# Kernel tuning notes

Hardware: AMD Instinct MI355X
Metric: run time of the kernel (lower is better)

The kernel has to match this reference:

```python
import jax, jax.numpy as jnp
import numpy as np

B, S, L = 32, 50, 16            # batch, seq_len, lectures per step
C, D = 50, 64                   # num_concepts, hidden_dim (key=value=summary dim)
NQ, NL, NU = 10000, 2000, 5000  # num_items, num_nonassessed_items, num_users
QV = NQ + NL + 1                # q_embed vocab (questions + lectures + pad)
QAV = 2 * NQ + 1                # qa_embed vocab
H4 = 4 * D                      # linear_dim = 4 * value_dim
EPS = 1e-5                      # torch LayerNorm default eps


def setup_inputs() -> dict:
    ks = jax.random.split(jax.random.key(0), 16)
    rn = lambda k, sh, sc: jax.random.normal(k, sh, jnp.float32) * sc
    return dict(
        q_data=jax.random.randint(ks[0], (B, S), 0, QV),
        qa_data=jax.random.randint(ks[1], (B, S), 0, QAV),
        l_data=jax.random.randint(ks[2], (B, S, L), 0, QV),
        users=jax.random.randint(ks[3], (B,), 0, NU + 1),
        key_matrix=rn(ks[4], (C, D), (2.0 / D) ** 0.5),   # key_matrix_embed rows 1..C (kaiming)
        q_embed=rn(ks[5], (QV, D), 0.02),
        qa_embed=rn(ks[6], (QAV, D), 0.02),
        u_embed=rn(ks[7], (NU + 1, D), 0.02),             # looked up but unused by write()
        M0=rn(ks[8], (C, D), (2.0 / D) ** 0.5),           # kaiming-init value matrix
        W_e=rn(ks[9], (D, D), D ** -0.5), b_e=jnp.zeros((D,), jnp.float32),
        W_a=rn(ks[10], (D, D), D ** -0.5), b_a=jnp.zeros((D,), jnp.float32),
        ln_gamma=jnp.ones((H4,), jnp.float32), ln_beta=jnp.zeros((H4,), jnp.float32),
        W0=rn(ks[11], (H4, H4), H4 ** -0.5), b0=jnp.zeros((H4,), jnp.float32),
        W1=rn(ks[12], (H4, H4), H4 ** -0.5), b1=jnp.zeros((H4,), jnp.float32),
        W_out=rn(ks[13], (H4, 1), H4 ** -0.5), b_out=jnp.zeros((1,), jnp.float32),
    )


def _forward(q_data, qa_data, l_data, key_matrix, q_embed, qa_embed, M0,
             W_e, b_e, W_a, b_a, ln_gamma, ln_beta, W0, b0, W1, b1, W_out, b_out):
    Bv = q_data.shape[0]
    q_e = q_embed[q_data]        # (B,S,D)
    qa_e = qa_embed[qa_data]     # (B,S,D)
    l_e = q_embed[l_data]        # (B,S,L,D) lectures share the q embedding table

    corr = lambda x: jax.nn.softmax(x @ key_matrix.T, axis=-1)  # softmax addressing
    q_cw = corr(q_e)             # (B,S,C)
    l_cw = corr(l_e)             # (B,S,L,C)
    # erase / add gates are memory-independent -> precompute (batched GEMMs)
    l_er = jax.nn.sigmoid(l_e @ W_e + b_e); l_ad = jnp.tanh(l_e @ W_a + b_a)
    q_er = jax.nn.sigmoid(qa_e @ W_e + b_e); q_ad = jnp.tanh(qa_e @ W_a + b_a)

    tm2 = lambda x: jnp.swapaxes(x, 0, 1)           # (B,S,..) -> (S,B,..)
    tm3 = lambda x: jnp.transpose(x, (1, 2, 0, 3))  # (B,S,L,..) -> (S,L,B,..)
    xs = (tm2(q_cw), tm2(q_e), tm2(q_er), tm2(q_ad),
          tm3(l_cw), tm3(l_e), tm3(l_er), tm3(l_ad))

    def write(M, w, e, a):  # erase-add gated write
        w = w[:, :, None]   # (B,C,1)
        return M * (1.0 - w * e[:, None, :]) + w * a[:, None, :]

    def layer_norm(x):
        mu = jnp.mean(x, -1, keepdims=True)
        v = jnp.var(x, -1, keepdims=True)
        return (x - mu) * jax.lax.rsqrt(v + EPS) * ln_gamma + ln_beta

    def outer(M, step):
        qcw, q, qer, qad, lcw, le, ler, lad = step
        q_read = jnp.einsum('bc,bcd->bd', qcw, M)  # read BEFORE lecture writes

        def inner(carry, lx):
            Mc, acc = carry
            w, e, a = lx
            acc = acc + jnp.einsum('bc,bcd->bd', w, Mc)  # read then write
            return (write(Mc, w, e, a), acc), None

        (M, l_read), _ = jax.lax.scan(inner, (M, jnp.zeros_like(q)), (lcw, ler, lad))
        # `l` after the loop is the LAST lecture embedding of this step
        mastery = layer_norm(jnp.concatenate([q_read, q, l_read, le[-1]], axis=-1))
        h = jax.nn.relu(mastery @ W0 + b0) @ W1 + b1   # dropout = identity (eval)
        pred = jax.nn.sigmoid(h @ W_out + b_out)[:, 0]
        M = write(M, qcw, qer, qad)                    # commit the q/a interaction
        return M, pred

    M_init = jnp.broadcast_to(M0, (Bv,) + M0.shape)
    _, preds = jax.lax.scan(outer, M_init, xs)
    return jnp.swapaxes(preds, 0, 1)                   # (B,S)


def reference(q_data, qa_data, l_data, users, key_matrix, q_embed, qa_embed,
              u_embed, M0, W_e, b_e, W_a, b_a, ln_gamma, ln_beta,
              W0, b0, W1, b1, W_out, b_out):
    # users/u_embed are looked up by the torch module but unused by write()'s math
    return _forward(q_data, qa_data, l_data, key_matrix, q_embed, qa_embed, M0,
                    W_e, b_e, W_a, b_a, ln_gamma, ln_beta, W0, b0, W1, b1, W_out, b_out)
```

## Files before the change

kernel.cpp:

```cpp
#include <hip/hip_runtime.h>
#include <math.h>

#define BB 32
#define SS 50
#define LL 16
#define CC 50
#define DD 64
#define NCH 13
#define H4 256
#define NROWS_Q (BB*SS)
#define NROWS_L (BB*SS*LL)

#define EA_ST 2176
#define W_ST  68

#define RB 64
#define NBLK_L (NROWS_L/RB)
#define NBLK_Q (NROWS_Q/RB)
#define NGB (NBLK_L + 2*NBLK_Q)

#define KBAT 16
#define NBAT (H4/KBAT)

static_assert(EA_ST == 17*128, "ea record: 17 slots x 64 lanes x float2");
static_assert(W_ST == 17*4, "w record: 17 slots x 4 chunk-cols");
static_assert(SS % 2 == 0, "phaseA double-step pipeline needs even SS");
static_assert(NROWS_L % RB == 0 && NROWS_Q % RB == 0, "GEMM row blocking");
static_assert(NBAT*KBAT == H4 && NBAT % 2 == 0,
              "phaseB k-loop must cover ALL of H4 in pairs of batches");
static_assert(SS*DD % 4 == 0, "phaseA partial copy uses float4");

#define OFF_EA     ((size_t)0)
#define OFF_W      (OFF_EA + (size_t)NROWS_Q*EA_ST)
#define OFF_PQP    (OFF_W  + (size_t)BB*NCH*SS*W_ST)
#define OFF_PLP    (OFF_PQP + (size_t)NCH*BB*SS*DD)
#define OFF_QE     (OFF_PLP + (size_t)NCH*BB*SS*DD)
#define OFF_LELAST (OFF_QE + (size_t)NROWS_Q*DD)

__global__ __launch_bounds__(256, 4) void k0_kernel(
    const int* __restrict__ qd, const int* __restrict__ qadx,
    const int* __restrict__ ld,
    const float* __restrict__ Kmat, const float* __restrict__ qemb,
    const float* __restrict__ qaemb,
    const float* __restrict__ We, const float* __restrict__ Wa,
    const float* __restrict__ be, const float* __restrict__ ba,
    float* __restrict__ eaW, float* __restrict__ wrecW,
    float* __restrict__ q_e_o, float* __restrict__ le_last)
{
    __shared__ float sX[RB*DD];
    __shared__ float sW[32*192];

    int tid = threadIdx.x;
    int bid = blockIdx.x;

    int bt, base;
    if (bid < NBLK_L)              { bt = 0; base = bid*RB; }
    else if (bid < NBLK_L+NBLK_Q)  { bt = 1; base = (bid-NBLK_L)*RB; }
    else                           { bt = 2; base = (bid-NBLK_L-NBLK_Q)*RB; }

    {
        const int*   idsrc = (bt==0) ? ld : (bt==1) ? qd : qadx;
        const float* tab   = (bt==2) ? qaemb : qemb;
        for (int idx = tid; idx < RB*16; idx += 256) {
            int r = idx >> 4, q = idx & 15;
            int id = idsrc[base + r];
            *(float4*)(sX + r*64 + q*4) =
                *(const float4*)(tab + (size_t)id*DD + q*4);
        }
    }

    auto stageW = [&](int kb) {
        #pragma unroll
        for (int n = 0; n < 4; ++n) {
            int f  = n*256 + tid;
            int kl = f >> 5, cf = f & 31;
            int k  = kb + kl;
            const float* src = (cf < 16) ? (We + k*64 + cf*4)
                                         : (Wa + k*64 + (cf-16)*4);
            *(float4*)(sW + kl*192 + cf*4) = *(const float4*)src;
        }
        #pragma unroll
        for (int n = 0; n < 8; ++n) {
            int f  = n*256 + tid;
            int kl = f >> 6, cr = f & 63;
            int k  = kb + kl;
            sW[kl*192 + 128 + cr] = (cr < CC) ? Kmat[cr*64 + k] : 0.f;
        }
    };

    int lane = tid & 63, wvi = tid >> 6;
    int r0 = wvi * 16;

    float accE[16], accA[16], accS[16];
    #pragma unroll
    for (int r = 0; r < 16; ++r) { accE[r] = 0.f; accA[r] = 0.f; accS[r] = 0.f; }

    stageW(0);
    __syncthreads();

    #pragma unroll 2
    for (int k4 = 0; k4 < 8; ++k4) {
        float wE[4], wA4[4], wS[4];
        #pragma unroll
        for (int kk = 0; kk < 4; ++kk) {
            int krow = (k4*4 + kk)*192;
            wE[kk]  = sW[krow + lane];
            wA4[kk] = sW[krow + 64 + lane];
            wS[kk]  = sW[krow + 128 + lane];
        }
        #pragma unroll
        for (int r = 0; r < 16; ++r) {
            float4 xv = *(const float4*)(sX + (r0+r)*64 + k4*4);
            accE[r] = fmaf(xv.x, wE[0], accE[r]);
            accE[r] = fmaf(xv.y, wE[1], accE[r]);
            accE[r] = fmaf(xv.z, wE[2], accE[r]);
            accE[r] = fmaf(xv.w, wE[3], accE[r]);
            accA[r] = fmaf(xv.x, wA4[0], accA[r]);
            accA[r] = fmaf(xv.y, wA4[1], accA[r]);
            accA[r] = fmaf(xv.z, wA4[2], accA[r]);
            accA[r] = fmaf(xv.w, wA4[3], accA[r]);
            accS[r] = fmaf(xv.x, wS[0], accS[r]);
            accS[r] = fmaf(xv.y, wS[1], accS[r]);
            accS[r] = fmaf(xv.z, wS[2], accS[r]);
            accS[r] = fmaf(xv.w, wS[3], accS[r]);
        }
    }
    __syncthreads();

    stageW(32);
    __syncthreads();

    #pragma unroll 2
    for (int k4 = 0; k4 < 8; ++k4) {
        float wE[4], wA4[4], wS[4];
        #pragma unroll
        for (int kk = 0; kk < 4; ++kk) {
            int krow = (k4*4 + kk)*192;
            wE[kk]  = sW[krow + lane];
            wA4[kk] = sW[krow + 64 + lane];
            wS[kk]  = sW[krow + 128 + lane];
        }
        #pragma unroll
        for (int r = 0; r < 16; ++r) {
            float4 xv = *(const float4*)(sX + (r0+r)*64 + 32 + k4*4);
            accE[r] = fmaf(xv.x, wE[0], accE[r]);
            accE[r] = fmaf(xv.y, wE[1], accE[r]);
            accE[r] = fmaf(xv.z, wE[2], accE[r]);
            accE[r] = fmaf(xv.w, wE[3], accE[r]);
            accA[r] = fmaf(xv.x, wA4[0], accA[r]);
            accA[r] = fmaf(xv.y, wA4[1], accA[r]);
            accA[r] = fmaf(xv.z, wA4[2], accA[r]);
            accA[r] = fmaf(xv.w, wA4[3], accA[r]);
            accS[r] = fmaf(xv.x, wS[0], accS[r]);
            accS[r] = fmaf(xv.y, wS[1], accS[r]);
            accS[r] = fmaf(xv.z, wS[2], accS[r]);
            accS[r] = fmaf(xv.w, wS[3], accS[r]);
        }
    }

    float bev = be[lane], bav = ba[lane];

    #pragma unroll
    for (int r = 0; r < 16; ++r) {
        int rr = r0 + r;
        int grow = base + rr;

        float s = (lane < CC) ? accS[r] : -1e30f;
        float mx = s;
        #pragma unroll
        for (int o = 32; o >= 1; o >>= 1) mx = fmaxf(mx, __shfl_xor(mx, o));
        float p = (lane < CC) ? expf(s - mx) : 0.f;
        float sum = p;
        #pragma unroll
        for (int o = 32; o >= 1; o >>= 1) sum += __shfl_xor(sum, o);
        float wsm = p / sum;

        if (bt == 0) {
            float erv = 1.f / (1.f + expf(-(accE[r] + bev)));
            float adv = tanhf(accA[r] + bav);
            int bs = grow >> 4, il = grow & 15;
            *(float2*)(eaW + (size_t)bs*EA_ST + il*128 + lane*2) =
                make_float2(erv, adv);
            int b = bs / SS, s2 = bs - b*SS;
            if (lane < 52) {
                int omx = lane >> 2, j = lane & 3;
                wrecW[(((size_t)(b*NCH + omx)*SS + s2)*17 + il)*4 + j] =
                    (lane < CC) ? wsm : 0.f;
            }
            if (il == LL-1) le_last[(size_t)bs*DD + lane] = sX[rr*64 + lane];
        } else if (bt == 1) {
            int qrow = grow;
            int b = qrow / SS, s2 = qrow - b*SS;
            if (lane < 52) {
                int omx = lane >> 2, j = lane & 3;
                wrecW[(((size_t)(b*NCH + omx)*SS + s2)*17 + 16)*4 + j] =
                    (lane < CC) ? wsm : 0.f;
            }
            q_e_o[(size_t)qrow*DD + lane] = sX[rr*64 + lane];
        } else {
            float erv = 1.f / (1.f + expf(-(accE[r] + bev)));
            float adv = tanhf(accA[r] + bav);
            int qrow = grow;
            *(float2*)(eaW + (size_t)qrow*EA_ST + 2048 + lane*2) =
                make_float2(erv, adv);
        }
    }
}

__global__ __launch_bounds__(64) void phaseA_kernel(
    const float* __restrict__ M0,
    const float* __restrict__ ea, const float* __restrict__ wrec,
    float* __restrict__ PqP, float* __restrict__ PlP)
{
    int om   = blockIdx.x >> 5;
    int b    = blockIdx.x & 31;
    int lane = threadIdx.x;
    int c0   = om * 4;

    __shared__ __align__(16) float wbuf[2][W_ST];
    __shared__ __align__(16) float sPq[SS*DD];
    __shared__ __align__(16) float sPl[SS*DD];

    float M[4];
    #pragma unroll
    for (int i = 0; i < 4; ++i) {
        int c = c0 + i;
        M[i] = (c < CC) ? M0[c*DD + lane] : 0.f;
    }

    const float* eb = ea   + (size_t)b*SS*EA_ST + lane*2;
    const float* wb = wrec + (size_t)(b*NCH + om)*SS*W_ST;

    float2 ea0[17], ea1[17];

    #pragma unroll
    for (int il = 0; il < 17; ++il)
        ea0[il] = *(const float2*)(eb + il*128);
    if (lane < 17)
        *(float4*)&wbuf[0][lane*4] = *(const float4*)(wb + lane*4);

    auto step = [&](int s, float2 (&cur)[17], float2 (&nxt)[17], int wbsel) {
        bool pf = (s < SS-1);
        float4 rw;
        if (pf) {
            const float* eg = eb + (size_t)(s+1)*EA_ST;
            #pragma unroll
            for (int il = 0; il < 17; ++il)
                nxt[il] = *(const float2*)(eg + il*128);
            if (lane < 17)
                rw = *(const float4*)(wb + (size_t)(s+1)*W_ST + lane*4);
        }

        float4 qw = *(const float4*)&wbuf[wbsel][64];
        float qr;
        qr = qw.x * M[0];
        qr = fmaf(qw.y, M[1], qr);
        qr = fmaf(qw.z, M[2], qr);
        qr = fmaf(qw.w, M[3], qr);

        float a0 = 0.f, a1 = 0.f, a2 = 0.f, a3 = 0.f;
        #pragma unroll
        for (int il = 0; il < 16; ++il) {
            float4 w = *(const float4*)&wbuf[wbsel][il*4];
            float e = cur[il].x, a = cur[il].y;
            a0 = fmaf(w.x, M[0], a0);
            a1 = fmaf(w.y, M[1], a1);
            a2 = fmaf(w.z, M[2], a2);
            a3 = fmaf(w.w, M[3], a3);
            M[0] = fmaf(w.x, fmaf(-e, M[0], a), M[0]);
            M[1] = fmaf(w.y, fmaf(-e, M[1], a), M[1]);
            M[2] = fmaf(w.z, fmaf(-e, M[2], a), M[2]);
            M[3] = fmaf(w.w, fmaf(-e, M[3], a), M[3]);
        }

        sPq[s*DD + lane] = qr;
        sPl[s*DD + lane] = (a0 + a1) + (a2 + a3);

        {
            float e = cur[16].x, a = cur[16].y;
            M[0] = fmaf(qw.x, fmaf(-e, M[0], a), M[0]);
            M[1] = fmaf(qw.y, fmaf(-e, M[1], a), M[1]);
            M[2] = fmaf(qw.z, fmaf(-e, M[2], a), M[2]);
            M[3] = fmaf(qw.w, fmaf(-e, M[3], a), M[3]);
        }

        if (pf && lane < 17)
            *(float4*)&wbuf[wbsel ^ 1][lane*4] = rw;
    };

    for (int s = 0; s < SS; s += 2) {
        step(s,     ea0, ea1, 0);
        step(s + 1, ea1, ea0, 1);
    }

    float* pqo = PqP + (size_t)(om*BB + b)*SS*DD;
    float* plo = PlP + (size_t)(om*BB + b)*SS*DD;
    for (int f = lane; f < SS*DD/4; f += 64) {
        *(float4*)(pqo + f*4) = *(const float4*)(sPq + f*4);
        *(float4*)(plo + f*4) = *(const float4*)(sPl + f*4);
    }
}

__global__ __launch_bounds__(256) void phaseB_kernel(
    const float* __restrict__ PqP, const float* __restrict__ PlP,
    const float* __restrict__ q_e_i, const float* __restrict__ le_last,
    const float* __restrict__ ln_g, const float* __restrict__ ln_b,
    const float* __restrict__ W0, const float* __restrict__ b0,
    const float* __restrict__ W1, const float* __restrict__ b1,
    const float* __restrict__ Wout, const float* __restrict__ bout,
    float* __restrict__ out)
{
    __shared__ float m[8][H4];
    __shared__ float h[8][H4];
    __shared__ float red[8][4];

    int j = threadIdx.x;
    int g0 = blockIdx.x * 8;
    int lane = j & 63, wv = j >> 6;

    int seg = j >> 6, dd = j & 63;
    #pragma unroll
    for (int r = 0; r < 8; ++r) {
        int g = g0 + r;
        float v;
        if (seg == 0) {
            v = 0.f;
            #pragma unroll
            for (int om = 0; om < NCH; ++om)
                v += PqP[((size_t)om*BB*SS + g)*DD + dd];
        } else if (seg == 1) {
            v = q_e_i[(size_t)g*DD + dd];
        } else if (seg == 2) {
            v = 0.f;
            #pragma unroll
            for (int om = 0; om < NCH; ++om)
                v += PlP[((size_t)om*BB*SS + g)*DD + dd];
        } else {
            v = le_last[(size_t)g*DD + dd];
        }
        m[r][j] = v;
    }
    __syncthreads();

    #pragma unroll
    for (int rr = 0; rr < 2; ++rr) {
        int r = wv + rr*4;
        float4 v4 = *(((const float4*)&m[r][0]) + lane);
        float s1 = v4.x + v4.y + v4.z + v4.w;
        float s2 = v4.x*v4.x + v4.y*v4.y + v4.z*v4.z + v4.w*v4.w;
        #pragma unroll
        for (int o = 32; o >= 1; o >>= 1) {
            s1 += __shfl_xor(s1, o);
            s2 += __shfl_xor(s2, o);
        }
        float mu  = s1 * (1.f/256.f);
        float var = s2 * (1.f/256.f) - mu*mu;
        float is  = rsqrtf(var + 1e-5f);
        float4 g4 = *(((const float4*)ln_g) + lane);
        float4 b4 = *(((const float4*)ln_b) + lane);
        float4 o4;
        o4.x = (v4.x - mu)*is*g4.x + b4.x;
        o4.y = (v4.y - mu)*is*g4.y + b4.y;
        o4.z = (v4.z - mu)*is*g4.z + b4.z;
        o4.w = (v4.w - mu)*is*g4.w + b4.w;
        *(((float4*)&m[r][0]) + lane) = o4;
    }
    __syncthreads();

    const float* Wp = W0 + j;
    float acc[8];
    {
        float bj = b0[j];
        #pragma unroll
        for (int r = 0; r < 8; ++r) acc[r] = bj;
    }
    {
        float wA[KBAT], wB[KBAT];
        #pragma unroll
        for (int t = 0; t < KBAT; ++t) wA[t] = Wp[(size_t)t*H4];
        #pragma unroll 1
        for (int kb = 0; kb < NBAT; kb += 2) {
            #pragma unroll
            for (int t = 0; t < KBAT; ++t)
                wB[t] = Wp[(size_t)((kb+1)*KBAT + t)*H4];
            #pragma unroll
            for (int t4 = 0; t4 < KBAT/4; ++t4) {
                #pragma unroll
                for (int r = 0; r < 8; ++r) {
                    float4 mv = *(const float4*)&m[r][kb*KBAT + t4*4];
                    acc[r] = fmaf(mv.x, wA[t4*4+0], acc[r]);
                    acc[r] = fmaf(mv.y, wA[t4*4+1], acc[r]);
                    acc[r] = fmaf(mv.z, wA[t4*4+2], acc[r]);
                    acc[r] = fmaf(mv.w, wA[t4*4+3], acc[r]);
                }
            }
            if (kb + 2 < NBAT) {
                #pragma unroll
                for (int t = 0; t < KBAT; ++t)
                    wA[t] = Wp[(size_t)((kb+2)*KBAT + t)*H4];
            }
            #pragma unroll
            for (int t4 = 0; t4 < KBAT/4; ++t4) {
                #pragma unroll
                for (int r = 0; r < 8; ++r) {
                    float4 mv = *(const float4*)&m[r][(kb+1)*KBAT + t4*4];
                    acc[r] = fmaf(mv.x, wB[t4*4+0], acc[r]);
                    acc[r] = fmaf(mv.y, wB[t4*4+1], acc[r]);
                    acc[r] = fmaf(mv.z, wB[t4*4+2], acc[r]);
                    acc[r] = fmaf(mv.w, wB[t4*4+3], acc[r]);
                }
            }
        }
    }
    #pragma unroll
    for (int r = 0; r < 8; ++r) h[r][j] = fmaxf(acc[r], 0.f);
    __syncthreads();

    const float* Wp1 = W1 + j;
    float a2[8];
    {
        float bj = b1[j];
        #pragma unroll
        for (int r = 0; r < 8; ++r) a2[r] = bj;
    }
    {
        float wA[KBAT], wB[KBAT];
        #pragma unroll
        for (int t = 0; t < KBAT; ++t) wA[t] = Wp1[(size_t)t*H4];
        #pragma unroll 1
        for (int kb = 0; kb < NBAT; kb += 2) {
            #pragma unroll
            for (int t = 0; t < KBAT; ++t)
                wB[t] = Wp1[(size_t)((kb+1)*KBAT + t)*H4];
            #pragma unroll
            for (int t4 = 0; t4 < KBAT/4; ++t4) {
                #pragma unroll
                for (int r = 0; r < 8; ++r) {
                    float4 hv = *(const float4*)&h[r][kb*KBAT + t4*4];
                    a2[r] = fmaf(hv.x, wA[t4*4+0], a2[r]);
                    a2[r] = fmaf(hv.y, wA[t4*4+1], a2[r]);
                    a2[r] = fmaf(hv.z, wA[t4*4+2], a2[r]);
                    a2[r] = fmaf(hv.w, wA[t4*4+3], a2[r]);
                }
            }
            if (kb + 2 < NBAT) {
                #pragma unroll
                for (int t = 0; t < KBAT; ++t)
                    wA[t] = Wp1[(size_t)((kb+2)*KBAT + t)*H4];
            }
            #pragma unroll
            for (int t4 = 0; t4 < KBAT/4; ++t4) {
                #pragma unroll
                for (int r = 0; r < 8; ++r) {
                    float4 hv = *(const float4*)&h[r][(kb+1)*KBAT + t4*4];
                    a2[r] = fmaf(hv.x, wB[t4*4+0], a2[r]);
                    a2[r] = fmaf(hv.y, wB[t4*4+1], a2[r]);
                    a2[r] = fmaf(hv.z, wB[t4*4+2], a2[r]);
                    a2[r] = fmaf(hv.w, wB[t4*4+3], a2[r]);
                }
            }
        }
    }

    float wo = Wout[j];
    #pragma unroll
    for (int r = 0; r < 8; ++r) {
        float v = a2[r] * wo;
        #pragma unroll
        for (int o = 32; o >= 1; o >>= 1) v += __shfl_xor(v, o);
        if (lane == 0) red[r][wv] = v;
    }
    __syncthreads();
    if (j < 8) {
        float t = red[j][0] + red[j][1] + red[j][2] + red[j][3] + bout[0];
        out[g0 + j] = 1.f / (1.f + expf(-t));
    }
}

extern "C" void kernel_launch(void* const* d_in, const int* in_sizes, int n_in,
                              void* d_out, int out_size, void* d_ws, size_t ws_size,
                              hipStream_t stream)
{
    const int*   q_data  = (const int*)  d_in[0];
    const int*   qa_data = (const int*)  d_in[1];
    const int*   l_data  = (const int*)  d_in[2];
    const float* Kmat    = (const float*)d_in[4];
    const float* q_embed = (const float*)d_in[5];
    const float* qa_embed= (const float*)d_in[6];
    const float* M0      = (const float*)d_in[8];
    const float* W_e     = (const float*)d_in[9];
    const float* b_e     = (const float*)d_in[10];
    const float* W_a     = (const float*)d_in[11];
    const float* b_a     = (const float*)d_in[12];
    const float* ln_g    = (const float*)d_in[13];
    const float* ln_b    = (const float*)d_in[14];
    const float* W0      = (const float*)d_in[15];
    const float* b0      = (const float*)d_in[16];
    const float* W1      = (const float*)d_in[17];
    const float* b1      = (const float*)d_in[18];
    const float* W_out   = (const float*)d_in[19];
    const float* b_out   = (const float*)d_in[20];

    float* ws = (float*)d_ws;
    float* eaW     = ws + OFF_EA;
    float* wrecW   = ws + OFF_W;
    float* PqP     = ws + OFF_PQP;
    float* PlP     = ws + OFF_PLP;
    float* q_e     = ws + OFF_QE;
    float* le_last = ws + OFF_LELAST;

    float* out = (float*)d_out;

    k0_kernel<<<NGB, 256, 0, stream>>>(q_data, qa_data, l_data,
                                       Kmat, q_embed, qa_embed,
                                       W_e, W_a, b_e, b_a,
                                       eaW, wrecW,
                                       q_e, le_last);
    phaseA_kernel<<<BB*NCH, 64, 0, stream>>>(M0, eaW, wrecW, PqP, PlP);
    phaseB_kernel<<<NROWS_Q/8, 256, 0, stream>>>(PqP, PlP, q_e, le_last,
                                                 ln_g, ln_b, W0, b0, W1, b1,
                                                 W_out, b_out, out);
}
```

Baseline: 199.4 us.

## Deepen phaseA prefetch to two steps ahead and halve k0 row block

```diff
diff --git a/kernel.cpp b/kernel.cpp
--- a/kernel.cpp
+++ b/kernel.cpp
@@ -14,7 +14,7 @@
 #define EA_ST 2176
 #define W_ST  68
 
-#define RB 64
+#define RB 32
 #define NBLK_L (NROWS_L/RB)
 #define NBLK_Q (NROWS_Q/RB)
 #define NGB (NBLK_L + 2*NBLK_Q)
@@ -24,8 +24,9 @@
 
 static_assert(EA_ST == 17*128, "ea record: 17 slots x 64 lanes x float2");
 static_assert(W_ST == 17*4, "w record: 17 slots x 4 chunk-cols");
-static_assert(SS % 2 == 0, "phaseA double-step pipeline needs even SS");
+static_assert(SS == 50, "phaseA pipeline is hand-unrolled for SS=50 (48+2)");
 static_assert(NROWS_L % RB == 0 && NROWS_Q % RB == 0, "GEMM row blocking");
+static_assert(RB % 16 == 0, "l-row il-groups must not straddle blocks");
 static_assert(NBAT*KBAT == H4 && NBAT % 2 == 0,
               "phaseB k-loop must cover ALL of H4 in pairs of batches");
 static_assert(SS*DD % 4 == 0, "phaseA partial copy uses float4");
@@ -89,11 +90,11 @@
     };
 
     int lane = tid & 63, wvi = tid >> 6;
-    int r0 = wvi * 16;
-
-    float accE[16], accA[16], accS[16];
-    #pragma unroll
-    for (int r = 0; r < 16; ++r) { accE[r] = 0.f; accA[r] = 0.f; accS[r] = 0.f; }
+    int r0 = wvi * 8;
+
+    float accE[8], accA[8], accS[8];
+    #pragma unroll
+    for (int r = 0; r < 8; ++r) { accE[r] = 0.f; accA[r] = 0.f; accS[r] = 0.f; }
 
     stageW(0);
     __syncthreads();
@@ -109,7 +110,7 @@
             wS[kk]  = sW[krow + 128 + lane];
         }
         #pragma unroll
-        for (int r = 0; r < 16; ++r) {
+        for (int r = 0; r < 8; ++r) {
             float4 xv = *(const float4*)(sX + (r0+r)*64 + k4*4);
             accE[r] = fmaf(xv.x, wE[0], accE[r]);
             accE[r] = fmaf(xv.y, wE[1], accE[r]);
@@ -141,7 +142,7 @@
             wS[kk]  = sW[krow + 128 + lane];
         }
         #pragma unroll
-        for (int r = 0; r < 16; ++r) {
+        for (int r = 0; r < 8; ++r) {
             float4 xv = *(const float4*)(sX + (r0+r)*64 + 32 + k4*4);
             accE[r] = fmaf(xv.x, wE[0], accE[r]);
             accE[r] = fmaf(xv.y, wE[1], accE[r]);
@@ -161,7 +162,7 @@
     float bev = be[lane], bav = ba[lane];
 
     #pragma unroll
-    for (int r = 0; r < 16; ++r) {
+    for (int r = 0; r < 8; ++r) {
         int rr = r0 + r;
         int grow = base + rr;
 
@@ -231,27 +232,34 @@
     const float* eb = ea   + (size_t)b*SS*EA_ST + lane*2;
     const float* wb = wrec + (size_t)(b*NCH + om)*SS*W_ST;
 
-    float2 ea0[17], ea1[17];
-
-    #pragma unroll
-    for (int il = 0; il < 17; ++il)
-        ea0[il] = *(const float2*)(eb + il*128);
-    if (lane < 17)
-        *(float4*)&wbuf[0][lane*4] = *(const float4*)(wb + lane*4);
-
-    auto step = [&](int s, float2 (&cur)[17], float2 (&nxt)[17], int wbsel) {
-        bool pf = (s < SS-1);
-        float4 rw;
-        if (pf) {
-            const float* eg = eb + (size_t)(s+1)*EA_ST;
+    float2 eaA[17], eaB[17], eaC[17];
+    float4 rw0, rw1, rw2;
+
+    #pragma unroll
+    for (int il = 0; il < 17; ++il) eaA[il] = *(const float2*)(eb + il*128);
+    #pragma unroll
+    for (int il = 0; il < 17; ++il) eaB[il] = *(const float2*)(eb + EA_ST + il*128);
+    if (lane < 17) {
+        float4 w0 = *(const float4*)(wb + lane*4);
+        *(float4*)&wbuf[0][lane*4] = w0;
+        rw0 = *(const float4*)(wb + (size_t)W_ST + lane*4);
+    }
+
+    auto step = [&](int s, float2 (&cur)[17], float2 (&nxt)[17],
+                    float4& rwW, float4& rwL, bool doLoad, bool doWrite) {
+        if (doLoad && lane < 17)
+            rwL = *(const float4*)(wb + (size_t)(s+2)*W_ST + lane*4);
+        if (doLoad) {
+            const float* eg = eb + (size_t)(s+2)*EA_ST;
             #pragma unroll
             for (int il = 0; il < 17; ++il)
                 nxt[il] = *(const float2*)(eg + il*128);
-            if (lane < 17)
-                rw = *(const float4*)(wb + (size_t)(s+1)*W_ST + lane*4);
-        }
-
-        float4 qw = *(const float4*)&wbuf[wbsel][64];
+        }
+        if (doWrite && lane < 17)
+            *(float4*)&wbuf[(s+1)&1][lane*4] = rwW;
+
+        const float* wbp = &wbuf[s&1][0];
+        float4 qw = *(const float4*)(wbp + 64);
         float qr;
         qr = qw.x * M[0];
         qr = fmaf(qw.y, M[1], qr);
@@ -261,7 +269,7 @@
         float a0 = 0.f, a1 = 0.f, a2 = 0.f, a3 = 0.f;
         #pragma unroll
         for (int il = 0; il < 16; ++il) {
-            float4 w = *(const float4*)&wbuf[wbsel][il*4];
+            float4 w = *(const float4*)(wbp + il*4);
             float e = cur[il].x, a = cur[il].y;
             a0 = fmaf(w.x, M[0], a0);
             a1 = fmaf(w.y, M[1], a1);
@@ -283,15 +291,15 @@
             M[2] = fmaf(qw.z, fmaf(-e, M[2], a), M[2]);
             M[3] = fmaf(qw.w, fmaf(-e, M[3], a), M[3]);
         }
-
-        if (pf && lane < 17)
-            *(float4*)&wbuf[wbsel ^ 1][lane*4] = rw;
     };
 
-    for (int s = 0; s < SS; s += 2) {
-        step(s,     ea0, ea1, 0);
-        step(s + 1, ea1, ea0, 1);
-    }
+    for (int s = 0; s < 48; s += 3) {
+        step(s,     eaA, eaC, rw0, rw1, true, true);
+        step(s + 1, eaB, eaA, rw1, rw2, true, true);
+        step(s + 2, eaC, eaB, rw2, rw0, true, true);
+    }
+    step(48, eaA, eaC, rw0, rw1, false, true);
+    step(49, eaB, eaA, rw1, rw2, false, false);
 
     float* pqo = PqP + (size_t)(om*BB + b)*SS*DD;
     float* plo = PlP + (size_t)(om*BB + b)*SS*DD;
```

After: 195.6 us. Within noise of the previous version (-1.9%).
